# Optimization experiments

Hardware: AMD Instinct MI355X
Metric: run time of the kernel (lower is better)

The kernel has to match this reference:

```python
import jax, jax.numpy as jnp
import numpy as np

N_NODES = 100000
N_EDGES = 1600000


def setup_inputs() -> dict:
    key = jax.random.key(0)
    ks = jax.random.split(key, 16)
    d_emb, d_mlp, d_lstm = 128, 256, 256
    B, C, T = 8, 4, 128
    return {
        "input_ids": jax.random.randint(ks[0], (B, C, T), 0, N_NODES, dtype=jnp.int64 if jax.config.jax_enable_x64 else jnp.int32),
        "input_mask": jnp.ones((B, C, T), dtype=jnp.int32),
        "labels": jax.random.uniform(ks[1], (B, C), dtype=jnp.float32),
        "src": jax.random.randint(ks[2], (N_EDGES,), 0, N_NODES),
        "dst": jax.random.randint(ks[3], (N_EDGES,), 0, N_NODES),
        "edge_value": jax.random.uniform(ks[4], (N_EDGES,), dtype=jnp.float32),
        "node_emb": jax.random.normal(ks[5], (N_NODES, d_emb), dtype=jnp.float32),
        "W1": jax.random.normal(ks[6], (d_mlp, d_emb), dtype=jnp.float32) * 0.05,
        "b1": jax.random.normal(ks[7], (d_mlp,), dtype=jnp.float32) * 0.05,
        "w_ih": jax.random.normal(ks[8], (4 * d_lstm, d_mlp), dtype=jnp.float32) * 0.05,
        "w_hh": jax.random.normal(ks[9], (4 * d_lstm, d_lstm), dtype=jnp.float32) * 0.05,
        "b_ih": jax.random.normal(ks[10], (4 * d_lstm,), dtype=jnp.float32) * 0.05,
        "b_hh": jax.random.normal(ks[11], (4 * d_lstm,), dtype=jnp.float32) * 0.05,
        "W2": jax.random.normal(ks[12], (1, d_lstm), dtype=jnp.float32) * 0.05,
        "b2": jax.random.normal(ks[13], (1,), dtype=jnp.float32) * 0.05,
    }


def reference(input_ids, input_mask, labels, src, dst, edge_value,
              node_emb, W1, b1, w_ih, w_hh, b_ih, b_hh, W2, b2):
    N = node_emb.shape[0]
    # edge-weighted mean message passing: u_mul_e('embedding','value') -> mean
    m = node_emb[src] * edge_value[:, None]                       # [E, d_emb]
    agg = jax.ops.segment_sum(m, dst, num_segments=N)             # [N, d_emb]
    cnt = jax.ops.segment_sum(jnp.ones_like(edge_value), dst, num_segments=N)
    h_nodes = agg / jnp.maximum(cnt, 1.0)[:, None]
    # linear1 on all nodes
    t_nodes = h_nodes @ W1.T + b1                                  # [N, d_mlp]
    B, C, T = input_ids.shape
    x = t_nodes[input_ids.reshape(B * C, T)]                       # [BC, T, d_mlp]
    lengths = input_mask.sum(axis=-1).reshape(B * C)               # [BC]
    H = w_hh.shape[1]

    def step(carry, xt):
        h, c = carry
        gates = xt @ w_ih.T + b_ih + h @ w_hh.T + b_hh
        i, f, g, o = jnp.split(gates, 4, axis=-1)  # torch LSTM gate order
        c = jax.nn.sigmoid(f) * c + jax.nn.sigmoid(i) * jnp.tanh(g)
        h = jax.nn.sigmoid(o) * jnp.tanh(c)
        return (h, c), h

    h0 = jnp.zeros((B * C, H), x.dtype)
    _, hs = jax.lax.scan(step, (h0, h0), jnp.swapaxes(x, 0, 1))    # [T, BC, H]
    hs = jnp.swapaxes(hs, 0, 1)                                    # [BC, T, H]
    idx = (lengths - 1).astype(jnp.int32)[:, None, None]
    h_last = jnp.take_along_axis(hs, jnp.broadcast_to(idx, (B * C, 1, H)), axis=1)[:, 0, :]
    scores = (h_last @ W2.T + b2).reshape(B, C)                    # [B, 4]
    p = jax.nn.softmax(scores, axis=1)
    # BCEWithLogits applied to softmaxed scores (as in the original)
    error = jnp.mean(jnp.maximum(p, 0) - p * labels + jnp.log1p(jnp.exp(-jnp.abs(p))))
    predictions = jnp.argmax(p, axis=1)
    return error, predictions
```

## Files before the change

kernel.cpp:

```cpp
#include <hip/hip_runtime.h>
#include <math.h>

#define NNODES 100000
#define NEDGES 1600000
#define NPOS   4096
#define NSEQ   32
#define TSTEPS 128
#define WRES   92

typedef float f32x4 __attribute__((ext_vector_type(4)));
typedef unsigned u32x4 __attribute__((ext_vector_type(4)));
typedef _Float16 h2v __attribute__((ext_vector_type(2)));

#define OFF_SLOT   0
#define OFF_AGG    400128
#define OFF_CNT    2497280
#define OFF_WF     2513664
#define OFF_BIASF  3037952
#define OFF_PREG   3042048
#define OFF_HS     19819264
#define OFF_WH16A  OFF_AGG
#define OFF_WH16L  (OFF_AGG + WRES * 1024 * 4)

static __device__ __forceinline__ float fdot2(unsigned w, unsigned h, float acc) {
#if __has_builtin(__builtin_amdgcn_fdot2)
  h2v wv, hv;
  __builtin_memcpy(&wv, &w, 4);
  __builtin_memcpy(&hv, &h, 4);
  return __builtin_amdgcn_fdot2(wv, hv, acc, false);
#else
  asm("v_dot2_f32_f16 %0, %1, %2, %0" : "+v"(acc) : "v"(w), "v"(h));
  return acc;
#endif
}

__global__ void k_init(int* slotmap, float* agg, float* cnt, float* hs0) {
  int i = blockIdx.x * blockDim.x + threadIdx.x;
  int stride = gridDim.x * blockDim.x;
  for (int idx = i; idx < 4096 * 128; idx += stride) agg[idx] = 0.f;
  for (int idx = i; idx < NNODES; idx += stride) slotmap[idx] = -1;
  for (int idx = i; idx < 4096; idx += stride) cnt[idx] = 0.f;
  for (int idx = i; idx < 8192; idx += stride) hs0[idx] = 0.f;
}

__global__ void k_mark(const int* __restrict__ input_ids, int* __restrict__ slotmap) {
  int p = blockIdx.x * blockDim.x + threadIdx.x;
  if (p < NPOS) atomicCAS(&slotmap[input_ids[p]], -1, p);
}

__global__ void k_edge(const int* __restrict__ src, const int* __restrict__ dst,
                       const float* __restrict__ ev, const float* __restrict__ emb,
                       const int* __restrict__ slotmap,
                       float* __restrict__ agg, float* __restrict__ cnt) {
  int e = blockIdx.x * 256 + threadIdx.x;
  int lane = threadIdx.x & 63;
  int d = dst[e];
  int slot = slotmap[d];
  int sn = 0; float vv = 0.f;
  if (slot >= 0) { sn = src[e]; vv = ev[e]; }
  unsigned long long m = __ballot(slot >= 0);
  while (m) {
    int j = __ffsll(m) - 1;
    m &= m - 1;
    int sl = __shfl(slot, j);
    int s2 = __shfl(sn, j);
    float v = __shfl(vv, j);
    float2 em = *(const float2*)&emb[(size_t)s2 * 128 + 2 * lane];
    atomicAdd(&agg[sl * 128 + 2 * lane],     em.x * v);
    atomicAdd(&agg[sl * 128 + 2 * lane + 1], em.y * v);
    if (lane == 0) atomicAdd(&cnt[sl], 1.f);
  }
}

__global__ void k_div(float* __restrict__ agg, const float* __restrict__ cnt) {
  int i = blockIdx.x * blockDim.x + threadIdx.x;
  agg[i] /= fmaxf(cnt[i >> 7], 1.f);
}

__global__ void k_fuse(const float* __restrict__ w_ih, const float* __restrict__ W1,
                       const float* __restrict__ b1, const float* __restrict__ b_ih,
                       const float* __restrict__ b_hh,
                       float* __restrict__ Wf, float* __restrict__ bf) {
  int row = blockIdx.x;
  int e = threadIdx.x;
  float acc = 0.f;
  for (int m2 = 0; m2 < 256; ++m2) acc += w_ih[row * 256 + m2] * W1[m2 * 128 + e];
  Wf[row * 128 + e] = acc;
  if (e == 0) {
    float bacc = b_ih[row] + b_hh[row];
    for (int m2 = 0; m2 < 256; ++m2) bacc += w_ih[row * 256 + m2] * b1[m2];
    bf[row] = bacc;
  }
}

__global__ __launch_bounds__(256, 2) void k_pregemm(
    const float* __restrict__ hnode, const float* __restrict__ Wf,
    const float* __restrict__ bf, const int* __restrict__ slotmap,
    const int* __restrict__ input_ids, float* __restrict__ preg) {
  __shared__ float Ash[64][132];
  __shared__ float Bsh[64][132];
  __shared__ int slots[64];
  int tid = threadIdx.x;
  int bm = (blockIdx.x & 63) * 64;
  int bn = (blockIdx.x >> 6) * 64;
  if (tid < 64) slots[tid] = slotmap[input_ids[bm + tid]];
  __syncthreads();
#pragma unroll
  for (int i = 0; i < 8; ++i) {
    int idx = tid + 256 * i;
    int r = idx >> 5, c = idx & 31;
    *(float4*)&Ash[r][c * 4] = *(const float4*)&hnode[slots[r] * 128 + c * 4];
    *(float4*)&Bsh[r][c * 4] = *(const float4*)&Wf[(bn + r) * 128 + c * 4];
  }
  __syncthreads();
  int tx = tid & 15, ty = tid >> 4;
  float acc[4][4] = {};
  for (int k = 0; k < 128; k += 4) {
    float4 a[4], bb[4];
#pragma unroll
    for (int i = 0; i < 4; ++i) a[i] = *(const float4*)&Ash[tx + 16 * i][k];
#pragma unroll
    for (int j = 0; j < 4; ++j) bb[j] = *(const float4*)&Bsh[ty + 16 * j][k];
#pragma unroll
    for (int i = 0; i < 4; ++i)
#pragma unroll
      for (int j = 0; j < 4; ++j)
        acc[i][j] += a[i].x * bb[j].x + a[i].y * bb[j].y + a[i].z * bb[j].z + a[i].w * bb[j].w;
  }
#pragma unroll
  for (int j = 0; j < 4; ++j) {
    int row = bn + ty + 16 * j;
    float bias = bf[row];
    int q  = row >> 8;
    int mm = (row >> 5) & 7;
    int dl = row & 31;
#pragma unroll
    for (int i = 0; i < 4; ++i) {
      int p = bm + tx + 16 * i;
      int s = p >> 7, tt = p & 127;
      preg[(((size_t)(tt * 32 + s) * 8 + mm) * 4 + q) * 32 + dl] = acc[i][j] + bias;
    }
  }
}

__global__ void k_wcvt(const float* __restrict__ w_hh,
                       unsigned* __restrict__ wRo, unsigned* __restrict__ wLo) {
  int idx = blockIdx.x * 256 + threadIdx.x;
  int row = idx >> 7;
  int j   = idx & 127;
  float x0 = w_hh[(size_t)row * 256 + 2 * j];
  float x1 = w_hh[(size_t)row * 256 + 2 * j + 1];
  union { _Float16 f[2]; unsigned u; } pk;
  pk.f[0] = (_Float16)x0;
  pk.f[1] = (_Float16)x1;
  int q = row >> 8, dd = row & 255;
  int kseg = j >> 5, p = j & 31;
  int tid = kseg * 256 + dd;
  if (q < 2) {
    wRo[(q * 32 + p) * 1024 + tid] = pk.u;
  } else if (q == 2 && p < 28) {
    wRo[(64 + p) * 1024 + tid] = pk.u;
  } else if (q == 2) {
    wLo[(0 * 1024 + tid) * 4 + (p - 28)] = pk.u;
  } else {
    wLo[((1 + (p >> 2)) * 1024 + tid) * 4 + (p & 3)] = pk.u;
  }
}

__global__ __launch_bounds__(1024) void k_lstm(
    const unsigned* __restrict__ wR, const unsigned* __restrict__ wLg,
    const float* __restrict__ preg, float* __restrict__ hs) {
  __shared__ __align__(16) unsigned whL[9 * 1024 * 4];
  __shared__ __align__(16) unsigned h16[128];
  __shared__ __align__(16) float    accb[3 * 256 * 4];
  const int tid  = threadIdx.x;
  const int s    = blockIdx.x;
  const int kseg = tid >> 8;
  const int d    = tid & 255;
  const bool owner = (kseg == 0);

  unsigned wv[WRES];
  {
    const unsigned* wa = wR + tid;
#pragma unroll
    for (int e = 0; e < WRES; ++e) wv[e] = wa[e * 1024];
#pragma unroll
    for (int e = 0; e < WRES; ++e) asm volatile("" : "+v"(wv[e]));
    const u32x4* srcL = (const u32x4*)wLg;
    u32x4* dstL = (u32x4*)whL;
#pragma unroll
    for (int j = 0; j < 9; ++j) dstL[j * 1024 + tid] = srcL[j * 1024 + tid];
  }
  if (tid < 128) h16[tid] = 0u;
  float c_st = 0.f;
  __syncthreads();

  const float* pregs = preg + ((size_t)s * 8 + (d >> 5)) * 128 + (d & 31);
  const u32x4* Lb   = (const u32x4*)whL + tid;
  const u32x4* hseg = (const u32x4*)h16 + kseg * 8;

  for (int t = 0; t < TSTEPS; ++t) {
    float pg0 = 0.f, pg1 = 0.f, pg2 = 0.f, pg3 = 0.f;
    if (owner) {
      const float* pb = pregs + (size_t)t * 32768;
      pg0 = pb[0]; pg1 = pb[32]; pg2 = pb[64]; pg3 = pb[96];
    }
    float a0 = 0.f, a1 = 0.f, a2 = 0.f, a3 = 0.f;
    u32x4 g2t = Lb[0];
#pragma unroll
    for (int c = 0; c < 8; ++c) {
      u32x4 h4 = hseg[c];
      u32x4 w3 = Lb[(1 + c) * 1024];
#pragma unroll
      for (int k = 0; k < 4; ++k) {
        a0 = fdot2(wv[c * 4 + k],      h4[k], a0);
        a1 = fdot2(wv[32 + c * 4 + k], h4[k], a1);
        a2 = fdot2(c < 7 ? wv[64 + c * 4 + k] : g2t[k], h4[k], a2);
        a3 = fdot2(w3[k],              h4[k], a3);
      }
    }
    if (!owner) {
      f32x4 r; r.x = a0; r.y = a1; r.z = a2; r.w = a3;
      *(f32x4*)&accb[((kseg - 1) * 256 + d) * 4] = r;
    }
    __syncthreads();
    if (owner) {
      f32x4 r0 = *(const f32x4*)&accb[(0 * 256 + d) * 4];
      f32x4 r1 = *(const f32x4*)&accb[(1 * 256 + d) * 4];
      f32x4 r2 = *(const f32x4*)&accb[(2 * 256 + d) * 4];
      float gi = a0 + r0.x + r1.x + r2.x + pg0;
      float gf = a1 + r0.y + r1.y + r2.y + pg1;
      float gg = a2 + r0.z + r1.z + r2.z + pg2;
      float go = a3 + r0.w + r1.w + r2.w + pg3;
      float si = 1.f / (1.f + expf(-gi));
      float sf = 1.f / (1.f + expf(-gf));
      float so = 1.f / (1.f + expf(-go));
      float cc = sf * c_st + si * tanhf(gg);
      float hh = so * tanhf(cc);
      c_st = cc;
      ((_Float16*)h16)[d] = (_Float16)hh;
      hs[(size_t)(t + 1) * 8192 + s * 256 + d] = hh;
    }
    __syncthreads();
  }
}

__global__ void k_final(const float* __restrict__ hs, const int* __restrict__ mask,
                        const float* __restrict__ labels, const float* __restrict__ W2,
                        const float* __restrict__ b2, float* __restrict__ out) {
  __shared__ float scores[32];
  __shared__ float errpart[8];
  int tid = threadIdx.x;
  if (tid < 32) {
    int len = 0;
    for (int t = 0; t < 128; ++t) len += mask[tid * 128 + t];
    if (len < 1) len = 1;
    const float* hl = hs + (size_t)len * 8192 + tid * 256;
    float acc = b2[0];
    for (int k = 0; k < 256; ++k) acc += hl[k] * W2[k];
    scores[tid] = acc;
  }
  __syncthreads();
  if (tid < 8) {
    float sc[4];
#pragma unroll
    for (int i = 0; i < 4; ++i) sc[i] = scores[tid * 4 + i];
    float mx = fmaxf(fmaxf(sc[0], sc[1]), fmaxf(sc[2], sc[3]));
    float ex[4], ssum = 0.f;
#pragma unroll
    for (int i = 0; i < 4; ++i) { ex[i] = expf(sc[i] - mx); ssum += ex[i]; }
    float esum = 0.f; int am = 0; float best = -1e30f;
#pragma unroll
    for (int i = 0; i < 4; ++i) {
      float p = ex[i] / ssum;
      float li = labels[tid * 4 + i];
      esum += fmaxf(p, 0.f) - p * li + log1pf(expf(-fabsf(p)));
      if (p > best) { best = p; am = i; }
    }
    errpart[tid] = esum;
    out[1 + tid] = (float)am;
  }
  __syncthreads();
  if (tid == 0) {
    float e = 0.f;
    for (int i = 0; i < 8; ++i) e += errpart[i];
    out[0] = e / 32.f;
  }
}

extern "C" void kernel_launch(void* const* d_in, const int* in_sizes, int n_in,
                              void* d_out, int out_size, void* d_ws, size_t ws_size,
                              hipStream_t stream) {
  const int*   input_ids  = (const int*)d_in[0];
  const int*   input_mask = (const int*)d_in[1];
  const float* labels     = (const float*)d_in[2];
  const int*   src        = (const int*)d_in[3];
  const int*   dst        = (const int*)d_in[4];
  const float* ev         = (const float*)d_in[5];
  const float* node_emb   = (const float*)d_in[6];
  const float* W1         = (const float*)d_in[7];
  const float* b1         = (const float*)d_in[8];
  const float* w_ih       = (const float*)d_in[9];
  const float* w_hh       = (const float*)d_in[10];
  const float* b_ih       = (const float*)d_in[11];
  const float* b_hh       = (const float*)d_in[12];
  const float* W2         = (const float*)d_in[13];
  const float* b2         = (const float*)d_in[14];
  float* out = (float*)d_out;
  char* ws = (char*)d_ws;
  int*      slotmap = (int*)(ws + OFF_SLOT);
  float*    agg     = (float*)(ws + OFF_AGG);
  float*    cnt     = (float*)(ws + OFF_CNT);
  float*    Wf      = (float*)(ws + OFF_WF);
  float*    biasf   = (float*)(ws + OFF_BIASF);
  float*    preg    = (float*)(ws + OFF_PREG);
  float*    hs      = (float*)(ws + OFF_HS);
  unsigned* wh16A   = (unsigned*)(ws + OFF_WH16A);
  unsigned* wh16L   = (unsigned*)(ws + OFF_WH16L);

  hipLaunchKernelGGL(k_init,    dim3(2048), dim3(256),  0, stream, slotmap, agg, cnt, hs);
  hipLaunchKernelGGL(k_mark,    dim3(16),   dim3(256),  0, stream, input_ids, slotmap);
  hipLaunchKernelGGL(k_edge,    dim3(6250), dim3(256),  0, stream, src, dst, ev, node_emb, slotmap, agg, cnt);
  hipLaunchKernelGGL(k_div,     dim3(2048), dim3(256),  0, stream, agg, cnt);
  hipLaunchKernelGGL(k_fuse,    dim3(1024), dim3(128),  0, stream, w_ih, W1, b1, b_ih, b_hh, Wf, biasf);
  hipLaunchKernelGGL(k_pregemm, dim3(1024), dim3(256),  0, stream, agg, Wf, biasf, slotmap, input_ids, preg);
  hipLaunchKernelGGL(k_wcvt,    dim3(512),  dim3(256),  0, stream, w_hh, wh16A, wh16L);
  hipLaunchKernelGGL(k_lstm,    dim3(NSEQ), dim3(1024), 0, stream, wh16A, wh16L, preg, hs);
  hipLaunchKernelGGL(k_final,   dim3(1),    dim3(64),   0, stream, hs, input_mask, labels, W2, b2, out);
}
```

Measured before the change: 334.9 us.

## Rebalance LSTM recurrent weights across registers, LDS and global streaming

Changes where the fp16 recurrent weight slices live in the LSTM kernel. Before, 92 words per thread were pinned in registers and 36 sat in shared memory. Now only 24 stay in registers, 36 stay in LDS, and the remaining 68 are re-read from global memory (L2/L1) at every timestep as 16-byte vectors. The aim is to free VGPRs and simplify the inner loop, at the cost of a large amount of per-step global memory traffic on the serial critical path.

```diff
diff --git a/kernel.cpp b/kernel.cpp
--- a/kernel.cpp
+++ b/kernel.cpp
@@ -6,7 +6,6 @@
 #define NPOS   4096
 #define NSEQ   32
 #define TSTEPS 128
-#define WRES   92
 
 typedef float f32x4 __attribute__((ext_vector_type(4)));
 typedef unsigned u32x4 __attribute__((ext_vector_type(4)));
@@ -19,8 +18,9 @@
 #define OFF_BIASF  3037952
 #define OFF_PREG   3042048
 #define OFF_HS     19819264
-#define OFF_WH16A  OFF_AGG
-#define OFF_WH16L  (OFF_AGG + WRES * 1024 * 4)
+#define OFF_WR  OFF_AGG
+#define OFF_WL  (OFF_AGG + 98304)
+#define OFF_WS  (OFF_AGG + 245760)
 
 static __device__ __forceinline__ float fdot2(unsigned w, unsigned h, float acc) {
 #if __has_builtin(__builtin_amdgcn_fdot2)
@@ -32,6 +32,14 @@
   asm("v_dot2_f32_f16 %0, %1, %2, %0" : "+v"(acc) : "v"(w), "v"(h));
   return acc;
 #endif
+}
+
+static __device__ __forceinline__ float dotq(u32x4 w, u32x4 h, float a) {
+  a = fdot2(w[0], h[0], a);
+  a = fdot2(w[1], h[1], a);
+  a = fdot2(w[2], h[2], a);
+  a = fdot2(w[3], h[3], a);
+  return a;
 }
 
 __global__ void k_init(int* slotmap, float* agg, float* cnt, float* hs0) {
@@ -143,8 +151,8 @@
   }
 }
 
-__global__ void k_wcvt(const float* __restrict__ w_hh,
-                       unsigned* __restrict__ wRo, unsigned* __restrict__ wLo) {
+__global__ void k_wcvt(const float* __restrict__ w_hh, unsigned* __restrict__ wR,
+                       unsigned* __restrict__ wL, unsigned* __restrict__ wS) {
   int idx = blockIdx.x * 256 + threadIdx.x;
   int row = idx >> 7;
   int j   = idx & 127;
@@ -155,21 +163,27 @@
   pk.f[1] = (_Float16)x1;
   int q = row >> 8, dd = row & 255;
   int kseg = j >> 5, p = j & 31;
+  int c = p >> 2, l = p & 3;
   int tid = kseg * 256 + dd;
-  if (q < 2) {
-    wRo[(q * 32 + p) * 1024 + tid] = pk.u;
-  } else if (q == 2 && p < 28) {
-    wRo[(64 + p) * 1024 + tid] = pk.u;
+  if (q == 0 && c < 6) {
+    wR[(c * 4 + l) * 1024 + tid] = pk.u;
+  } else if (q == 0) {
+    wL[((c - 6) * 1024 + tid) * 4 + l] = pk.u;
+  } else if (q == 1 && c < 7) {
+    wL[((2 + c) * 1024 + tid) * 4 + l] = pk.u;
+  } else if (q == 1) {
+    wS[(14 * 1024 + tid) * 4 + l] = pk.u;
   } else if (q == 2) {
-    wLo[(0 * 1024 + tid) * 4 + (p - 28)] = pk.u;
+    wS[(((c < 7) ? (2 * c) : 15) * 1024 + tid) * 4 + l] = pk.u;
   } else {
-    wLo[((1 + (p >> 2)) * 1024 + tid) * 4 + (p & 3)] = pk.u;
+    wS[(((c < 7) ? (2 * c + 1) : 16) * 1024 + tid) * 4 + l] = pk.u;
   }
 }
 
 __global__ __launch_bounds__(1024) void k_lstm(
-    const unsigned* __restrict__ wR, const unsigned* __restrict__ wLg,
-    const float* __restrict__ preg, float* __restrict__ hs) {
+    const unsigned* __restrict__ wR, const unsigned* __restrict__ wL,
+    const unsigned* __restrict__ wS, const float* __restrict__ preg,
+    float* __restrict__ hs) {
   __shared__ __align__(16) unsigned whL[9 * 1024 * 4];
   __shared__ __align__(16) unsigned h16[128];
   __shared__ __align__(16) float    accb[3 * 256 * 4];
@@ -179,45 +193,47 @@
   const int d    = tid & 255;
   const bool owner = (kseg == 0);
 
-  unsigned wv[WRES];
+  u32x4 rq[6];
+#pragma unroll
+  for (int qr = 0; qr < 6; ++qr)
+#pragma unroll
+    for (int l = 0; l < 4; ++l)
+      rq[qr][l] = wR[(qr * 4 + l) * 1024 + tid];
   {
-    const unsigned* wa = wR + tid;
-#pragma unroll
-    for (int e = 0; e < WRES; ++e) wv[e] = wa[e * 1024];
-#pragma unroll
-    for (int e = 0; e < WRES; ++e) asm volatile("" : "+v"(wv[e]));
-    const u32x4* srcL = (const u32x4*)wLg;
-    u32x4* dstL = (u32x4*)whL;
-#pragma unroll
-    for (int j = 0; j < 9; ++j) dstL[j * 1024 + tid] = srcL[j * 1024 + tid];
+    const u32x4* src = (const u32x4*)wL;
+    u32x4* dst = (u32x4*)whL;
+#pragma unroll
+    for (int lc = 0; lc < 9; ++lc)
+      dst[lc * 1024 + tid] = src[lc * 1024 + tid];
   }
   if (tid < 128) h16[tid] = 0u;
   float c_st = 0.f;
   __syncthreads();
 
-  const float* pregs = preg + ((size_t)s * 8 + (d >> 5)) * 128 + (d & 31);
-  const u32x4* Lb   = (const u32x4*)whL + tid;
-  const u32x4* hseg = (const u32x4*)h16 + kseg * 8;
+  const u32x4* hqp = (const u32x4*)h16 + kseg * 8;
+  const u32x4* lq  = (const u32x4*)whL + tid;
+  const u32x4* sq  = (const u32x4*)wS + tid;
 
   for (int t = 0; t < TSTEPS; ++t) {
-    float pg0 = 0.f, pg1 = 0.f, pg2 = 0.f, pg3 = 0.f;
+    float pg[4] = {0.f, 0.f, 0.f, 0.f};
     if (owner) {
-      const float* pb = pregs + (size_t)t * 32768;
-      pg0 = pb[0]; pg1 = pb[32]; pg2 = pb[64]; pg3 = pb[96];
+      const float* pb = preg + (((size_t)(t * 32 + s) * 8 + (d >> 5)) * 4) * 32
+                        + (d & 31);
+#pragma unroll
+      for (int q = 0; q < 4; ++q) pg[q] = pb[q * 32];
     }
     float a0 = 0.f, a1 = 0.f, a2 = 0.f, a3 = 0.f;
-    u32x4 g2t = Lb[0];
 #pragma unroll
     for (int c = 0; c < 8; ++c) {
-      u32x4 h4 = hseg[c];
-      u32x4 w3 = Lb[(1 + c) * 1024];
-#pragma unroll
-      for (int k = 0; k < 4; ++k) {
-        a0 = fdot2(wv[c * 4 + k],      h4[k], a0);
-        a1 = fdot2(wv[32 + c * 4 + k], h4[k], a1);
-        a2 = fdot2(c < 7 ? wv[64 + c * 4 + k] : g2t[k], h4[k], a2);
-        a3 = fdot2(w3[k],              h4[k], a3);
-      }
+      u32x4 h4 = hqp[c];
+      u32x4 w0 = (c < 6) ? rq[c] : lq[(c - 6) * 1024];
+      u32x4 w1 = (c < 7) ? lq[(2 + c) * 1024] : sq[14 * 1024];
+      u32x4 w2 = sq[((c < 7) ? (2 * c) : 15) * 1024];
+      u32x4 w3 = sq[((c < 7) ? (2 * c + 1) : 16) * 1024];
+      a0 = dotq(w0, h4, a0);
+      a1 = dotq(w1, h4, a1);
+      a2 = dotq(w2, h4, a2);
+      a3 = dotq(w3, h4, a3);
     }
     if (!owner) {
       f32x4 r; r.x = a0; r.y = a1; r.z = a2; r.w = a3;
@@ -228,10 +244,10 @@
       f32x4 r0 = *(const f32x4*)&accb[(0 * 256 + d) * 4];
       f32x4 r1 = *(const f32x4*)&accb[(1 * 256 + d) * 4];
       f32x4 r2 = *(const f32x4*)&accb[(2 * 256 + d) * 4];
-      float gi = a0 + r0.x + r1.x + r2.x + pg0;
-      float gf = a1 + r0.y + r1.y + r2.y + pg1;
-      float gg = a2 + r0.z + r1.z + r2.z + pg2;
-      float go = a3 + r0.w + r1.w + r2.w + pg3;
+      float gi = a0 + r0.x + r1.x + r2.x + pg[0];
+      float gf = a1 + r0.y + r1.y + r2.y + pg[1];
+      float gg = a2 + r0.z + r1.z + r2.z + pg[2];
+      float go = a3 + r0.w + r1.w + r2.w + pg[3];
       float si = 1.f / (1.f + expf(-gi));
       float sf = 1.f / (1.f + expf(-gf));
       float so = 1.f / (1.f + expf(-go));
@@ -315,8 +331,9 @@
   float*    biasf   = (float*)(ws + OFF_BIASF);
   float*    preg    = (float*)(ws + OFF_PREG);
   float*    hs      = (float*)(ws + OFF_HS);
-  unsigned* wh16A   = (unsigned*)(ws + OFF_WH16A);
-  unsigned* wh16L   = (unsigned*)(ws + OFF_WH16L);
+  unsigned* wRimg   = (unsigned*)(ws + OFF_WR);
+  unsigned* wLimg   = (unsigned*)(ws + OFF_WL);
+  unsigned* wSimg   = (unsigned*)(ws + OFF_WS);
 
   hipLaunchKernelGGL(k_init,    dim3(2048), dim3(256),  0, stream, slotmap, agg, cnt, hs);
   hipLaunchKernelGGL(k_mark,    dim3(16),   dim3(256),  0, stream, input_ids, slotmap);
@@ -324,7 +341,7 @@
   hipLaunchKernelGGL(k_div,     dim3(2048), dim3(256),  0, stream, agg, cnt);
   hipLaunchKernelGGL(k_fuse,    dim3(1024), dim3(128),  0, stream, w_ih, W1, b1, b_ih, b_hh, Wf, biasf);
   hipLaunchKernelGGL(k_pregemm, dim3(1024), dim3(256),  0, stream, agg, Wf, biasf, slotmap, input_ids, preg);
-  hipLaunchKernelGGL(k_wcvt,    dim3(512),  dim3(256),  0, stream, w_hh, wh16A, wh16L);
-  hipLaunchKernelGGL(k_lstm,    dim3(NSEQ), dim3(1024), 0, stream, wh16A, wh16L, preg, hs);
+  hipLaunchKernelGGL(k_wcvt,    dim3(512),  dim3(256),  0, stream, w_hh, wRimg, wLimg, wSimg);
+  hipLaunchKernelGGL(k_lstm,    dim3(NSEQ), dim3(1024), 0, stream, wRimg, wLimg, wSimg, preg, hs);
   hipLaunchKernelGGL(k_final,   dim3(1),    dim3(64),   0, stream, hs, input_mask, labels, W2, b2, out);
 }
```

Measured after the change: 334.0 us (median of 2 runs). Within noise of the previous version (-0.3%).
